# Kernel tuning notes

Hardware: AMD Instinct MI355X
Metric: run time of the kernel (lower is better)

Reference implementation:

```python
import jax, jax.numpy as jnp
import numpy as np

IGNORE_LABEL = 255
THRESH = 0.7
MIN_KEPT = 262144


def setup_inputs() -> dict:
    key = jax.random.key(0)
    k1, k2 = jax.random.split(key)
    pred = jax.random.normal(k1, (8, 19, 768, 768), dtype=jnp.float32)
    target = jax.random.randint(k2, (8, 768, 768), 0, 19, dtype=jnp.int32)
    return {"pred": pred, "target": target}


def reference(pred, target):
    b, c, h, w = pred.shape
    n = b * h * w

    t = target.reshape(-1)                      # [N]
    valid = t != IGNORE_LABEL                   # [N] bool
    tc = jnp.where(valid, t, 0)                 # clamp ignored labels to 0 for gather
    num_valid = valid.sum()

    # pred.transpose(0,1).reshape(c,-1) in torch flattens (b,h,w) b-major,
    # matching target.view(-1); here we use [N, C] layout instead.
    logits = jnp.transpose(pred, (0, 2, 3, 1)).reshape(n, c)  # [N, C]
    logp = jax.nn.log_softmax(logits, axis=-1)                # [N, C]
    logp_t = jnp.take_along_axis(logp, tc[:, None], axis=-1)[:, 0]  # [N]

    # prob of the ground-truth class; invalid pixels masked to 1 (never "hard")
    mask_prob = jnp.where(valid, jnp.exp(logp_t), 1.0)        # [N]

    # k-th smallest gt-prob defines the OHEM threshold (raised if > thresh)
    k = min(n, MIN_KEPT)
    kth = jnp.sort(mask_prob)[k - 1]
    threshold = jnp.maximum(kth, THRESH)
    kept = mask_prob <= threshold

    # torch: OHEM applies only when min_kept <= num_valid and num_valid > 0
    do_ohem = (num_valid > 0) & (num_valid >= MIN_KEPT)
    valid_f = jnp.where(do_ohem, valid & kept, valid)

    # CrossEntropyLoss(reduction='mean', ignore_index=ignore_label)
    pix_loss = -logp_t                                        # [N]
    denom = jnp.maximum(valid_f.sum(), 1).astype(pred.dtype)
    loss = jnp.sum(jnp.where(valid_f, pix_loss, 0.0)) / denom
    return loss
```

## Files before the change

### kernel.cpp

```cpp
#include <hip/hip_runtime.h>


#define BB 8
#define CC 19
#define HH 768
#define WW 768
#define HWSZ (HH * WW)
#define NPIX (BB * HWSZ)
#define KSEL 262144
#define IGNORE_LBL 255
#define THR 0.7f

#define HIST1_OFF 8
#define HIST2_OFF (HIST1_OFF + 2048)
#define HIST3_OFF (HIST2_OFF + 2048)
#define META_WORDS 8192
#define PROB_OFF META_WORDS

__global__ __launch_bounds__(256) void k_init(unsigned* __restrict__ ws) {
    for (int i = threadIdx.x; i < META_WORDS; i += 256) ws[i] = 0u;
}

__global__ __launch_bounds__(256) void k_pass1(const float* __restrict__ pred,
                                               const int* __restrict__ target,
                                               unsigned* __restrict__ ws,
                                               float* __restrict__ logp_out,
                                               int has_logp) {
    __shared__ unsigned hist[2048];
    __shared__ unsigned snv;
    for (int i = threadIdx.x; i < 2048; i += 256) hist[i] = 0u;
    if (threadIdx.x == 0) snv = 0u;
    __syncthreads();

    int g = blockIdx.x * 256 + threadIdx.x;
    int pix0 = g * 4;
    int b = pix0 / HWSZ;
    int hw = pix0 - b * HWSZ;
    const float* base = pred + (size_t)b * ((size_t)CC * HWSZ) + hw;

    float x[CC][4];
#pragma unroll
    for (int c = 0; c < CC; ++c) {
        float4 v = *reinterpret_cast<const float4*>(base + (size_t)c * HWSZ);
        x[c][0] = v.x; x[c][1] = v.y; x[c][2] = v.z; x[c][3] = v.w;
    }
    int4 t4 = *reinterpret_cast<const int4*>(target + pix0);
    int tt[4] = {t4.x, t4.y, t4.z, t4.w};

    unsigned pbits[4];
    float plogp[4];
    int nv = 0;
#pragma unroll
    for (int p = 0; p < 4; ++p) {
        int t = tt[p];
        bool valid = (t != IGNORE_LBL);
        nv += valid ? 1 : 0;
        int tc = valid ? t : 0;
        float m = x[0][p];
#pragma unroll
        for (int c = 1; c < CC; ++c) m = fmaxf(m, x[c][p]);
        float s = 0.0f;
        float xt = x[0][p];
#pragma unroll
        for (int c = 0; c < CC; ++c) {
            float v = x[c][p];
            s += expf(v - m);
            xt = (c == tc) ? v : xt;
        }
        float lp = xt - m - logf(s);
        float pr = valid ? expf(lp) : 1.0f;
        pbits[p] = __float_as_uint(pr);
        plogp[p] = lp;
        atomicAdd(&hist[pbits[p] >> 21], 1u);
    }
    *reinterpret_cast<uint4*>(ws + PROB_OFF + pix0) =
        make_uint4(pbits[0], pbits[1], pbits[2], pbits[3]);
    if (has_logp)
        *reinterpret_cast<float4*>(logp_out + pix0) =
            make_float4(plogp[0], plogp[1], plogp[2], plogp[3]);
    atomicAdd(&snv, (unsigned)nv);
    __syncthreads();
    for (int i = threadIdx.x; i < 2048; i += 256) {
        unsigned v = hist[i];
        if (v) atomicAdd(ws + HIST1_OFF + i, v);
    }
    if (threadIdx.x == 0) atomicAdd(ws + 0, snv);
}

__global__ __launch_bounds__(256) void k_scan(unsigned* __restrict__ ws, int level) {
    const unsigned* hist;
    int nbins, shift;
    if (level == 1)      { hist = ws + HIST1_OFF; nbins = 2048; shift = 21; }
    else if (level == 2) { hist = ws + HIST2_OFF; nbins = 2048; shift = 10; }
    else                 { hist = ws + HIST3_OFF; nbins = 1024; shift = 0;  }
    int chunk = nbins >> 8;
    int t = threadIdx.x;
    __shared__ unsigned csum[256];
    unsigned s = 0;
    for (int j = 0; j < chunk; ++j) s += hist[t * chunk + j];
    csum[t] = s;
    unsigned krem = (level == 1) ? (unsigned)KSEL : ws[1];
    unsigned selprev = (level == 1) ? 0u : ws[2];
    unsigned nvv = ws[0];
    for (int off = 1; off < 256; off <<= 1) {
        __syncthreads();
        unsigned add = (t >= off) ? csum[t - off] : 0u;
        __syncthreads();
        csum[t] += add;
    }
    unsigned incl = csum[t];
    unsigned excl = incl - s;
    bool own = (excl < krem) && (krem <= incl);
    __syncthreads();
    if (own) {
        unsigned running = excl;
        int bin = 0;
        unsigned cb = excl;
        for (int j = 0; j < chunk; ++j) {
            unsigned h = hist[t * chunk + j];
            if (running + h >= krem) { bin = t * chunk + j; cb = running; break; }
            running += h;
        }
        unsigned sel = selprev | (((unsigned)bin) << shift);
        ws[2] = sel;
        ws[1] = krem - cb;
        if (level == 3) {
            float kth = __uint_as_float(sel);
            reinterpret_cast<float*>(ws)[5] = fmaxf(kth, THR);
            ws[4] = (nvv > 0u && nvv >= (unsigned)KSEL) ? 1u : 0u;
        }
    }
}

__global__ __launch_bounds__(256) void k_refine(unsigned* __restrict__ ws, int level) {
    __shared__ unsigned hist[2048];
    int nb = (level == 2) ? 2048 : 1024;
    for (int i = threadIdx.x; i < nb; i += 256) hist[i] = 0u;
    __syncthreads();
    unsigned sel = ws[2];
    const uint4* pb = reinterpret_cast<const uint4*>(ws + PROB_OFF);
    int idx = blockIdx.x * 256 + threadIdx.x;
    const int stride = 1152 * 256;
#pragma unroll
    for (int it = 0; it < 4; ++it) {
        uint4 v = pb[idx + it * stride];
        unsigned arr[4] = {v.x, v.y, v.z, v.w};
#pragma unroll
        for (int p = 0; p < 4; ++p) {
            unsigned bits = arr[p];
            if (level == 2) {
                if ((bits >> 21) == (sel >> 21))
                    atomicAdd(&hist[(bits >> 10) & 2047u], 1u);
            } else {
                if ((bits >> 10) == (sel >> 10))
                    atomicAdd(&hist[bits & 1023u], 1u);
            }
        }
    }
    __syncthreads();
    unsigned* gh = ws + ((level == 2) ? HIST2_OFF : HIST3_OFF);
    for (int i = threadIdx.x; i < nb; i += 256) {
        unsigned v = hist[i];
        if (v) atomicAdd(gh + i, v);
    }
}

__global__ __launch_bounds__(256) void k_final(unsigned* __restrict__ ws,
                                               const float* __restrict__ logp,
                                               const int* __restrict__ target,
                                               int has_logp) {
    float thr = __uint_as_float(ws[5]);
    unsigned do_ohem = ws[4];
    int g = blockIdx.x * 256 + threadIdx.x;
    int pix0 = g * 4;
    uint4 pv = *reinterpret_cast<const uint4*>(ws + PROB_OFF + pix0);
    int4 t4 = *reinterpret_cast<const int4*>(target + pix0);
    float4 lp4 = make_float4(0.f, 0.f, 0.f, 0.f);
    if (has_logp) lp4 = *reinterpret_cast<const float4*>(logp + pix0);
    unsigned pb[4] = {pv.x, pv.y, pv.z, pv.w};
    int tt[4] = {t4.x, t4.y, t4.z, t4.w};
    float lpv[4] = {lp4.x, lp4.y, lp4.z, lp4.w};
    float ls = 0.0f;
    unsigned lc = 0;
#pragma unroll
    for (int p = 0; p < 4; ++p) {
        bool valid = (tt[p] != IGNORE_LBL);
        float pr = __uint_as_float(pb[p]);
        bool kept = (pr <= thr);
        bool vf = do_ohem ? (valid && kept) : valid;
        float pl = has_logp ? (-lpv[p]) : (-logf(fmaxf(pr, 1e-37f)));
        if (vf) { ls += pl; lc += 1u; }
    }
    __shared__ float ssum;
    __shared__ unsigned scnt;
    if (threadIdx.x == 0) { ssum = 0.0f; scnt = 0u; }
    __syncthreads();
    for (int off = 32; off > 0; off >>= 1) {
        ls += __shfl_down(ls, off);
        lc += __shfl_down(lc, off);
    }
    if ((threadIdx.x & 63) == 0) {
        atomicAdd(&ssum, ls);
        atomicAdd(&scnt, lc);
    }
    __syncthreads();
    if (threadIdx.x == 0) {
        atomicAdd(reinterpret_cast<double*>(ws + 6), (double)ssum);
        atomicAdd(ws + 3, scnt);
    }
}

__global__ void k_finalize(const unsigned* __restrict__ ws, float* __restrict__ out) {
    if (threadIdx.x == 0 && blockIdx.x == 0) {
        double s = *reinterpret_cast<const double*>(ws + 6);
        unsigned c = ws[3];
        unsigned d = (c > 0u) ? c : 1u;
        out[0] = (float)(s / (double)d);
    }
}

extern "C" void kernel_launch(void* const* d_in, const int* in_sizes, int n_in,
                              void* d_out, int out_size, void* d_ws, size_t ws_size,
                              hipStream_t stream) {
    const float* pred = (const float*)d_in[0];
    const int* target = (const int*)d_in[1];
    unsigned* ws = (unsigned*)d_ws;
    float* out = (float*)d_out;

    size_t need_full = ((size_t)META_WORDS + (size_t)NPIX) * 4u + (size_t)NPIX * 4u;
    int has_logp = (ws_size >= need_full) ? 1 : 0;
    float* logp = reinterpret_cast<float*>(ws + META_WORDS + NPIX);

    k_init<<<1, 256, 0, stream>>>(ws);
    k_pass1<<<NPIX / 1024, 256, 0, stream>>>(pred, target, ws, logp, has_logp);
    k_scan<<<1, 256, 0, stream>>>(ws, 1);
    k_refine<<<1152, 256, 0, stream>>>(ws, 2);
    k_scan<<<1, 256, 0, stream>>>(ws, 2);
    k_refine<<<1152, 256, 0, stream>>>(ws, 3);
    k_scan<<<1, 256, 0, stream>>>(ws, 3);
    k_final<<<NPIX / 1024, 256, 0, stream>>>(ws, logp, target, has_logp);
    k_finalize<<<1, 64, 0, stream>>>(ws, out);
}
```

Baseline: 626.6 us.

## Fuse histogram scans into consumer kernels and drop stored log-prob buffer

Removes the three single-block scan kernels by having every block of the refine and final kernels recompute the radix-select bin from the global histograms. The per-pixel log-prob output buffer is dropped; the final pass recomputes the loss as -log(prob). Pass1, refine and final now use a fixed grid of 1152 blocks that each loop over four chunks, and global histogram flushes are rotated per block to spread atomic contention. The cost is redundant per-block prefix scans, plus small precision differences from recomputing log of a stored probability.

```diff
diff --git a/kernel.cpp b/kernel.cpp
--- a/kernel.cpp
+++ b/kernel.cpp
@@ -1,15 +1,14 @@
 #include <hip/hip_runtime.h>
 
 
-#define BB 8
 #define CC 19
-#define HH 768
-#define WW 768
-#define HWSZ (HH * WW)
-#define NPIX (BB * HWSZ)
+#define HWSZ 589824
+#define NPIX 4718592
 #define KSEL 262144
 #define IGNORE_LBL 255
 #define THR 0.7f
+#define NBLK 1152
+#define ITERS 4
 
 #define HIST1_OFF 8
 #define HIST2_OFF (HIST1_OFF + 2048)
@@ -21,87 +20,20 @@
     for (int i = threadIdx.x; i < META_WORDS; i += 256) ws[i] = 0u;
 }
 
-__global__ __launch_bounds__(256) void k_pass1(const float* __restrict__ pred,
-                                               const int* __restrict__ target,
-                                               unsigned* __restrict__ ws,
-                                               float* __restrict__ logp_out,
-                                               int has_logp) {
-    __shared__ unsigned hist[2048];
-    __shared__ unsigned snv;
-    for (int i = threadIdx.x; i < 2048; i += 256) hist[i] = 0u;
-    if (threadIdx.x == 0) snv = 0u;
-    __syncthreads();
-
-    int g = blockIdx.x * 256 + threadIdx.x;
-    int pix0 = g * 4;
-    int b = pix0 / HWSZ;
-    int hw = pix0 - b * HWSZ;
-    const float* base = pred + (size_t)b * ((size_t)CC * HWSZ) + hw;
-
-    float x[CC][4];
-#pragma unroll
-    for (int c = 0; c < CC; ++c) {
-        float4 v = *reinterpret_cast<const float4*>(base + (size_t)c * HWSZ);
-        x[c][0] = v.x; x[c][1] = v.y; x[c][2] = v.z; x[c][3] = v.w;
-    }
-    int4 t4 = *reinterpret_cast<const int4*>(target + pix0);
-    int tt[4] = {t4.x, t4.y, t4.z, t4.w};
-
-    unsigned pbits[4];
-    float plogp[4];
-    int nv = 0;
-#pragma unroll
-    for (int p = 0; p < 4; ++p) {
-        int t = tt[p];
-        bool valid = (t != IGNORE_LBL);
-        nv += valid ? 1 : 0;
-        int tc = valid ? t : 0;
-        float m = x[0][p];
-#pragma unroll
-        for (int c = 1; c < CC; ++c) m = fmaxf(m, x[c][p]);
-        float s = 0.0f;
-        float xt = x[0][p];
-#pragma unroll
-        for (int c = 0; c < CC; ++c) {
-            float v = x[c][p];
-            s += expf(v - m);
-            xt = (c == tc) ? v : xt;
-        }
-        float lp = xt - m - logf(s);
-        float pr = valid ? expf(lp) : 1.0f;
-        pbits[p] = __float_as_uint(pr);
-        plogp[p] = lp;
-        atomicAdd(&hist[pbits[p] >> 21], 1u);
-    }
-    *reinterpret_cast<uint4*>(ws + PROB_OFF + pix0) =
-        make_uint4(pbits[0], pbits[1], pbits[2], pbits[3]);
-    if (has_logp)
-        *reinterpret_cast<float4*>(logp_out + pix0) =
-            make_float4(plogp[0], plogp[1], plogp[2], plogp[3]);
-    atomicAdd(&snv, (unsigned)nv);
-    __syncthreads();
-    for (int i = threadIdx.x; i < 2048; i += 256) {
-        unsigned v = hist[i];
-        if (v) atomicAdd(ws + HIST1_OFF + i, v);
-    }
-    if (threadIdx.x == 0) atomicAdd(ws + 0, snv);
-}
-
-__global__ __launch_bounds__(256) void k_scan(unsigned* __restrict__ ws, int level) {
-    const unsigned* hist;
-    int nbins, shift;
-    if (level == 1)      { hist = ws + HIST1_OFF; nbins = 2048; shift = 21; }
-    else if (level == 2) { hist = ws + HIST2_OFF; nbins = 2048; shift = 10; }
-    else                 { hist = ws + HIST3_OFF; nbins = 1024; shift = 0;  }
-    int chunk = nbins >> 8;
-    int t = threadIdx.x;
+template <int NBINS>
+__device__ __forceinline__ void find_bin(const unsigned* __restrict__ gh,
+                                         unsigned krem_in, int shift,
+                                         unsigned& sel_io, unsigned& krem_out) {
+    constexpr int CHUNK = NBINS / 256;
     __shared__ unsigned csum[256];
+    __shared__ unsigned sb[2];
+    const int t = threadIdx.x;
+    __syncthreads();
+    unsigned loc[CHUNK];
     unsigned s = 0;
-    for (int j = 0; j < chunk; ++j) s += hist[t * chunk + j];
+#pragma unroll
+    for (int j = 0; j < CHUNK; ++j) { loc[j] = gh[t * CHUNK + j]; s += loc[j]; }
     csum[t] = s;
-    unsigned krem = (level == 1) ? (unsigned)KSEL : ws[1];
-    unsigned selprev = (level == 1) ? 0u : ws[2];
-    unsigned nvv = ws[0];
     for (int off = 1; off < 256; off <<= 1) {
         __syncthreads();
         unsigned add = (t >= off) ? csum[t - off] : 0u;
@@ -110,45 +42,105 @@
     }
     unsigned incl = csum[t];
     unsigned excl = incl - s;
-    bool own = (excl < krem) && (krem <= incl);
-    __syncthreads();
-    if (own) {
-        unsigned running = excl;
-        int bin = 0;
-        unsigned cb = excl;
-        for (int j = 0; j < chunk; ++j) {
-            unsigned h = hist[t * chunk + j];
-            if (running + h >= krem) { bin = t * chunk + j; cb = running; break; }
-            running += h;
-        }
-        unsigned sel = selprev | (((unsigned)bin) << shift);
-        ws[2] = sel;
-        ws[1] = krem - cb;
-        if (level == 3) {
-            float kth = __uint_as_float(sel);
-            reinterpret_cast<float*>(ws)[5] = fmaxf(kth, THR);
-            ws[4] = (nvv > 0u && nvv >= (unsigned)KSEL) ? 1u : 0u;
-        }
-    }
-}
-
-__global__ __launch_bounds__(256) void k_refine(unsigned* __restrict__ ws, int level) {
+    if (excl < krem_in && krem_in <= incl) {
+        unsigned run = excl;
+        unsigned bin = 0;
+        bool found = false;
+#pragma unroll
+        for (int j = 0; j < CHUNK; ++j) {
+            unsigned nrun = run + loc[j];
+            if (!found && nrun >= krem_in) { bin = (unsigned)(t * CHUNK + j); found = true; }
+            if (!found) run = nrun;
+        }
+        sb[0] = bin;
+        sb[1] = krem_in - run;
+    }
+    __syncthreads();
+    sel_io |= sb[0] << shift;
+    krem_out = sb[1];
+}
+
+__global__ __launch_bounds__(256) void k_pass1(const float* __restrict__ pred,
+                                               const int* __restrict__ target,
+                                               unsigned* __restrict__ ws) {
     __shared__ unsigned hist[2048];
-    int nb = (level == 2) ? 2048 : 1024;
-    for (int i = threadIdx.x; i < nb; i += 256) hist[i] = 0u;
-    __syncthreads();
-    unsigned sel = ws[2];
-    const uint4* pb = reinterpret_cast<const uint4*>(ws + PROB_OFF);
-    int idx = blockIdx.x * 256 + threadIdx.x;
-    const int stride = 1152 * 256;
-#pragma unroll
-    for (int it = 0; it < 4; ++it) {
-        uint4 v = pb[idx + it * stride];
-        unsigned arr[4] = {v.x, v.y, v.z, v.w};
+    for (int i = threadIdx.x; i < 2048; i += 256) hist[i] = 0u;
+    __syncthreads();
+
+    unsigned nv = 0;
+    for (int it = 0; it < ITERS; ++it) {
+        int q = it * (NBLK * 256) + blockIdx.x * 256 + threadIdx.x;
+        int pix0 = q * 4;
+        int b = pix0 / HWSZ;
+        int hw = pix0 - b * HWSZ;
+        const float* base = pred + (size_t)b * ((size_t)CC * HWSZ) + hw;
+
+        float x[CC][4];
+#pragma unroll
+        for (int c = 0; c < CC; ++c) {
+            float4 v = *reinterpret_cast<const float4*>(base + (size_t)c * HWSZ);
+            x[c][0] = v.x; x[c][1] = v.y; x[c][2] = v.z; x[c][3] = v.w;
+        }
+        int4 t4 = *reinterpret_cast<const int4*>(target + pix0);
+        int tt[4] = {t4.x, t4.y, t4.z, t4.w};
+
+        unsigned pb[4];
 #pragma unroll
         for (int p = 0; p < 4; ++p) {
-            unsigned bits = arr[p];
-            if (level == 2) {
+            int t = tt[p];
+            bool valid = (t != IGNORE_LBL);
+            nv += valid ? 1u : 0u;
+            int tc = valid ? t : 0;
+            float m = x[0][p];
+#pragma unroll
+            for (int c = 1; c < CC; ++c) m = fmaxf(m, x[c][p]);
+            float s = 0.0f;
+            float xt = x[0][p];
+#pragma unroll
+            for (int c = 0; c < CC; ++c) {
+                float v = x[c][p];
+                s += expf(v - m);
+                xt = (c == tc) ? v : xt;
+            }
+            float lp = xt - m - logf(s);
+            float pr = valid ? expf(lp) : 1.0f;
+            pb[p] = __float_as_uint(pr);
+            atomicAdd(&hist[pb[p] >> 21], 1u);
+        }
+        *reinterpret_cast<uint4*>(ws + PROB_OFF + pix0) =
+            make_uint4(pb[0], pb[1], pb[2], pb[3]);
+    }
+
+    for (int off = 32; off; off >>= 1) nv += __shfl_down(nv, off);
+    if ((threadIdx.x & 63) == 0) atomicAdd(ws + 0, nv);
+
+    __syncthreads();
+    int rot = (blockIdx.x & 7) << 8;
+    for (int i = threadIdx.x; i < 2048; i += 256) {
+        int idx = (i + rot) & 2047;
+        unsigned v = hist[idx];
+        if (v) atomicAdd(ws + HIST1_OFF + idx, v);
+    }
+}
+
+template <int LEVEL>
+__global__ __launch_bounds__(256) void k_refine(unsigned* __restrict__ ws) {
+    constexpr int NB = (LEVEL == 2) ? 2048 : 1024;
+    __shared__ unsigned hist[NB];
+    for (int i = threadIdx.x; i < NB; i += 256) hist[i] = 0u;
+    unsigned sel = 0, krem = 0;
+    find_bin<2048>(ws + HIST1_OFF, (unsigned)KSEL, 21, sel, krem);
+    if (LEVEL == 3) find_bin<2048>(ws + HIST2_OFF, krem, 10, sel, krem);
+
+    const uint4* pbv = reinterpret_cast<const uint4*>(ws + PROB_OFF);
+    for (int it = 0; it < ITERS; ++it) {
+        int q = it * (NBLK * 256) + blockIdx.x * 256 + threadIdx.x;
+        uint4 v = pbv[q];
+        unsigned a[4] = {v.x, v.y, v.z, v.w};
+#pragma unroll
+        for (int p = 0; p < 4; ++p) {
+            unsigned bits = a[p];
+            if (LEVEL == 2) {
                 if ((bits >> 21) == (sel >> 21))
                     atomicAdd(&hist[(bits >> 10) & 2047u], 1u);
             } else {
@@ -158,55 +150,60 @@
         }
     }
     __syncthreads();
-    unsigned* gh = ws + ((level == 2) ? HIST2_OFF : HIST3_OFF);
-    for (int i = threadIdx.x; i < nb; i += 256) {
-        unsigned v = hist[i];
-        if (v) atomicAdd(gh + i, v);
+    unsigned* gh = ws + ((LEVEL == 2) ? HIST2_OFF : HIST3_OFF);
+    int rot = (blockIdx.x & 3) << 8;
+    for (int i = threadIdx.x; i < NB; i += 256) {
+        int idx = (i + rot) & (NB - 1);
+        unsigned v = hist[idx];
+        if (v) atomicAdd(gh + idx, v);
     }
 }
 
 __global__ __launch_bounds__(256) void k_final(unsigned* __restrict__ ws,
-                                               const float* __restrict__ logp,
-                                               const int* __restrict__ target,
-                                               int has_logp) {
-    float thr = __uint_as_float(ws[5]);
-    unsigned do_ohem = ws[4];
-    int g = blockIdx.x * 256 + threadIdx.x;
-    int pix0 = g * 4;
-    uint4 pv = *reinterpret_cast<const uint4*>(ws + PROB_OFF + pix0);
-    int4 t4 = *reinterpret_cast<const int4*>(target + pix0);
-    float4 lp4 = make_float4(0.f, 0.f, 0.f, 0.f);
-    if (has_logp) lp4 = *reinterpret_cast<const float4*>(logp + pix0);
-    unsigned pb[4] = {pv.x, pv.y, pv.z, pv.w};
-    int tt[4] = {t4.x, t4.y, t4.z, t4.w};
-    float lpv[4] = {lp4.x, lp4.y, lp4.z, lp4.w};
+                                               const int* __restrict__ target) {
+    unsigned sel = 0, krem = 0;
+    find_bin<2048>(ws + HIST1_OFF, (unsigned)KSEL, 21, sel, krem);
+    find_bin<2048>(ws + HIST2_OFF, krem, 10, sel, krem);
+    find_bin<1024>(ws + HIST3_OFF, krem, 0, sel, krem);
+    float thr = fmaxf(__uint_as_float(sel), THR);
+    unsigned nvv = ws[0];
+    bool do_ohem = (nvv > 0u) && (nvv >= (unsigned)KSEL);
+
+    const uint4* pbv = reinterpret_cast<const uint4*>(ws + PROB_OFF);
     float ls = 0.0f;
     unsigned lc = 0;
-#pragma unroll
-    for (int p = 0; p < 4; ++p) {
-        bool valid = (tt[p] != IGNORE_LBL);
-        float pr = __uint_as_float(pb[p]);
-        bool kept = (pr <= thr);
-        bool vf = do_ohem ? (valid && kept) : valid;
-        float pl = has_logp ? (-lpv[p]) : (-logf(fmaxf(pr, 1e-37f)));
-        if (vf) { ls += pl; lc += 1u; }
-    }
-    __shared__ float ssum;
-    __shared__ unsigned scnt;
-    if (threadIdx.x == 0) { ssum = 0.0f; scnt = 0u; }
-    __syncthreads();
-    for (int off = 32; off > 0; off >>= 1) {
+    for (int it = 0; it < ITERS; ++it) {
+        int q = it * (NBLK * 256) + blockIdx.x * 256 + threadIdx.x;
+        int pix0 = q * 4;
+        uint4 v = pbv[q];
+        int4 t4 = *reinterpret_cast<const int4*>(target + pix0);
+        unsigned a[4] = {v.x, v.y, v.z, v.w};
+        int tt[4] = {t4.x, t4.y, t4.z, t4.w};
+#pragma unroll
+        for (int p = 0; p < 4; ++p) {
+            bool valid = (tt[p] != IGNORE_LBL);
+            float pr = __uint_as_float(a[p]);
+            bool kept = (pr <= thr);
+            bool vf = do_ohem ? (valid && kept) : valid;
+            if (vf) { ls += -logf(pr); lc += 1u; }
+        }
+    }
+    for (int off = 32; off; off >>= 1) {
         ls += __shfl_down(ls, off);
         lc += __shfl_down(lc, off);
     }
+    __shared__ float wsum[4];
+    __shared__ unsigned wcnt[4];
     if ((threadIdx.x & 63) == 0) {
-        atomicAdd(&ssum, ls);
-        atomicAdd(&scnt, lc);
+        wsum[threadIdx.x >> 6] = ls;
+        wcnt[threadIdx.x >> 6] = lc;
     }
     __syncthreads();
     if (threadIdx.x == 0) {
-        atomicAdd(reinterpret_cast<double*>(ws + 6), (double)ssum);
-        atomicAdd(ws + 3, scnt);
+        float bs = wsum[0] + wsum[1] + wsum[2] + wsum[3];
+        unsigned bc = wcnt[0] + wcnt[1] + wcnt[2] + wcnt[3];
+        atomicAdd(reinterpret_cast<double*>(ws + 6), (double)bs);
+        atomicAdd(ws + 3, bc);
     }
 }
 
@@ -227,17 +224,10 @@
     unsigned* ws = (unsigned*)d_ws;
     float* out = (float*)d_out;
 
-    size_t need_full = ((size_t)META_WORDS + (size_t)NPIX) * 4u + (size_t)NPIX * 4u;
-    int has_logp = (ws_size >= need_full) ? 1 : 0;
-    float* logp = reinterpret_cast<float*>(ws + META_WORDS + NPIX);
-
     k_init<<<1, 256, 0, stream>>>(ws);
-    k_pass1<<<NPIX / 1024, 256, 0, stream>>>(pred, target, ws, logp, has_logp);
-    k_scan<<<1, 256, 0, stream>>>(ws, 1);
-    k_refine<<<1152, 256, 0, stream>>>(ws, 2);
-    k_scan<<<1, 256, 0, stream>>>(ws, 2);
-    k_refine<<<1152, 256, 0, stream>>>(ws, 3);
-    k_scan<<<1, 256, 0, stream>>>(ws, 3);
-    k_final<<<NPIX / 1024, 256, 0, stream>>>(ws, logp, target, has_logp);
+    k_pass1<<<NBLK, 256, 0, stream>>>(pred, target, ws);
+    k_refine<2><<<NBLK, 256, 0, stream>>>(ws);
+    k_refine<3><<<NBLK, 256, 0, stream>>>(ws);
+    k_final<<<NBLK, 256, 0, stream>>>(ws, target);
     k_finalize<<<1, 64, 0, stream>>>(ws, out);
 }
```

After: 579.7 us. -7.5%, faster.
